# Kernel tuning notes

Measured on AMD Instinct MI355X. Metric: run time of the kernel, lower is better.

The kernel has to match this reference:

```python
import jax, jax.numpy as jnp
import numpy as np
from jax import lax

K = 3  # AdaConv kernel_size inside conv_block


def conv2d(x, w, b, pad):
    # x: (B,C,H,W), w: (O,I,kh,kw) -> NCHW conv with symmetric padding
    y = lax.conv_general_dilated(x, w, (1, 1), [(pad, pad), (pad, pad)],
                                 dimension_numbers=('NCHW', 'OIHW', 'NCHW'))
    return y + b[None, :, None, None]


def unfold3(x):
    # nn.Unfold(kernel=3, pad=1): patches ordered channel-major then (kh,kw) row-major
    B, C, H, W = x.shape
    xp = jnp.pad(x, ((0, 0), (0, 0), (1, 1), (1, 1)))
    return jnp.stack([xp[:, :, i:i + H, j:j + W]
                      for i in range(K) for j in range(K)], axis=2)  # (B,C,9,H,W)


def adaconv(x, mask, aw_w, aw_b, mt_w, mt_b, c_w, c_b):
    # groups=1, groups_channels=out_ch in this configuration
    weight = conv2d(mask, aw_w, aw_b, pad=2)          # (B, 9, H, W)
    x = conv2d(x, c_w, c_b, pad=1)                    # (B, out_ch, H, W)
    p = unfold3(x)                                    # (B, out_ch, 9, H, W)
    out = jnp.einsum('bkhw,bckhw->bchw', weight, p)   # per-pixel adaptive conv
    mask2 = conv2d(mask, mt_w, mt_b, pad=2)
    return out, mask2


def lrelu(x):
    return jax.nn.leaky_relu(x, 0.01)


def setup_inputs() -> dict:
    key = jax.random.key(0)
    ks = jax.random.split(key, 20)
    B, Cin, Cout, Mi, Mo, H, W = 2, 64, 64, 64, 64, 256, 256
    s = 0.05
    d = {
        'x': jax.random.normal(ks[0], (B, Cin, H, W), jnp.float32),
        'mask': jax.random.normal(ks[1], (B, Mi, H, W), jnp.float32),
        # AdaConv 1 (in_ch->out_ch, mask_in->mask_out)
        'aw1_w': jax.random.normal(ks[2], (K * K, Mi, 2 * K - 1, 2 * K - 1), jnp.float32) * s,
        'aw1_b': jax.random.normal(ks[3], (K * K,), jnp.float32) * s,
        'mt1_w': jax.random.normal(ks[4], (Mo, Mi, 2 * K - 1, 2 * K - 1), jnp.float32) * s,
        'mt1_b': jax.random.normal(ks[5], (Mo,), jnp.float32) * s,
        'c1_w': jax.random.normal(ks[6], (Cout, Cin, K, K), jnp.float32) * s,
        'c1_b': jax.random.normal(ks[7], (Cout,), jnp.float32) * s,
        # AdaConv 2 (out_ch->out_ch, mask_out->mask_out)
        'aw2_w': jax.random.normal(ks[8], (K * K, Mo, 2 * K - 1, 2 * K - 1), jnp.float32) * s,
        'aw2_b': jax.random.normal(ks[9], (K * K,), jnp.float32) * s,
        'mt2_w': jax.random.normal(ks[10], (Mo, Mo, 2 * K - 1, 2 * K - 1), jnp.float32) * s,
        'mt2_b': jax.random.normal(ks[11], (Mo,), jnp.float32) * s,
        'c2_w': jax.random.normal(ks[12], (Cout, Cout, K, K), jnp.float32) * s,
        'c2_b': jax.random.normal(ks[13], (Cout,), jnp.float32) * s,
        # 1x1 residual conv
        'cr_w': jax.random.normal(ks[14], (Cout, Cin, 1, 1), jnp.float32) * s,
        'cr_b': jax.random.normal(ks[15], (Cout,), jnp.float32) * s,
    }
    return d


def reference(x, mask, aw1_w, aw1_b, mt1_w, mt1_b, c1_w, c1_b,
              aw2_w, aw2_b, mt2_w, mt2_b, c2_w, c2_b, cr_w, cr_b):
    res = conv2d(x, cr_w, cr_b, pad=0)
    x, mask = adaconv(x, mask, aw1_w, aw1_b, mt1_w, mt1_b, c1_w, c1_b)
    x, mask = lrelu(x), lrelu(mask)
    x, mask = adaconv(x, mask, aw2_w, aw2_b, mt2_w, mt2_b, c2_w, c2_b)
    x, mask = lrelu(x), lrelu(mask)
    return (x + res, mask)
```

## Files before the change

kernel.cpp:

```cpp
#include <hip/hip_runtime.h>

#define HWSZ 65536
#define CCH  64

typedef __bf16 bf16x8 __attribute__((ext_vector_type(8)));
typedef __bf16 bf16x4 __attribute__((ext_vector_type(4)));
typedef float  f32x4  __attribute__((ext_vector_type(4)));

__device__ inline void gload_lds16(const void* g, void* l) {
    __builtin_amdgcn_global_load_lds(
        (const __attribute__((address_space(1))) void*)g,
        (__attribute__((address_space(3))) void*)l, 16, 0, 0);
}


__device__ void cvt_body(int cb, const float* __restrict__ src,
                         __bf16* __restrict__ dst)
{
    int p  = cb * 256 + threadIdx.x;
    int b  = p >> 16, hw = p & 65535;
    const float* sp = src + (((size_t)b * 64) << 16) + hw;
    __bf16* dp = dst + (size_t)p * 64;
    #pragma unroll
    for (int c8 = 0; c8 < 8; ++c8) {
        bf16x8 v8;
        #pragma unroll
        for (int j = 0; j < 8; ++j)
            v8[j] = (__bf16)sp[(size_t)(c8 * 8 + j) << 16];
        *(bf16x8*)(dp + c8 * 8) = v8;
    }
}

__device__ void prep3_body(int cb, const float* __restrict__ src,
                           __bf16* __restrict__ dst)
{
    int t = cb * 256 + threadIdx.x;
    if (t >= 2 * 9 * 2048) return;
    int j  = t & 7;
    int u  = (t >> 3) & 255;
    int q  = t >> 11;
    int k  = q % 9, ci = q / 9;
    int r  = u >> 3;
    int v  = (u & 7) ^ (r & 7);
    int o  = 2 * r + (v >> 2);
    int g  = v & 3;
    int i  = ci * 32 + g * 8 + j;
    dst[t] = (__bf16)src[((size_t)o * 64 + i) * 9 + k];
}

__device__ void prep1_body(int cb, const float* __restrict__ src,
                           __bf16* __restrict__ dst)
{
    int t = cb * 256 + threadIdx.x;
    if (t >= 2 * 2048) return;
    int j  = t & 7;
    int u  = (t >> 3) & 255;
    int ci = t >> 11;
    int r  = u >> 3;
    int v  = (u & 7) ^ (r & 7);
    int o  = 2 * r + (v >> 2);
    int g  = v & 3;
    int i  = ci * 32 + g * 8 + j;
    dst[t] = (__bf16)src[(size_t)o * 64 + i];
}

__device__ void prepF_body(int cb, const float* __restrict__ mt,
                           const float* __restrict__ aw, __bf16* __restrict__ dst)
{
    int t = cb * 256 + threadIdx.x;
    if (t >= 2 * 25 * 3072) return;
    int j  = t & 7;
    int u  = (t >> 3) % 384;
    int q  = t / 3072;
    int k  = q % 25, ci = q / 25;
    int r  = u >> 3;
    int v  = (u & 7) ^ (r & 7);
    int o  = 2 * r + (v >> 2);
    int g  = v & 3;
    int i  = ci * 32 + g * 8 + j;
    float val = 0.f;
    if (o < 64)      val = mt[((size_t)o * 64 + i) * 25 + k];
    else if (o < 73) val = aw[((size_t)(o - 64) * 64 + i) * 25 + k];
    dst[t] = (__bf16)val;
}

__global__ __launch_bounds__(256) void k_prep(
    const float* x, const float* mask,
    const float* c1w, const float* c2w,
    const float* mt1w, const float* aw1w,
    const float* mt2w, const float* aw2w,
    const float* crw,
    __bf16* xh, __bf16* mh,
    __bf16* wbc1, __bf16* wbc2, __bf16* wbF1, __bf16* wbF2, __bf16* wbcr)
{
    int bid = blockIdx.x;
    if      (bid < 512)  cvt_body(bid, x, xh);
    else if (bid < 1024) cvt_body(bid - 512, mask, mh);
    else if (bid < 1168) prep3_body(bid - 1024, c1w, wbc1);
    else if (bid < 1312) prep3_body(bid - 1168, c2w, wbc2);
    else if (bid < 1912) prepF_body(bid - 1312, mt1w, aw1w, wbF1);
    else if (bid < 2512) prepF_body(bid - 1912, mt2w, aw2w, wbF2);
    else                 prep1_body(bid - 2512, crw, wbcr);
}

template<int EPI>
__global__ __launch_bounds__(256) void k_conv5(
    const __bf16* __restrict__ xh, const __bf16* __restrict__ wb,
    const float* __restrict__ bias, const float* __restrict__ bias2,
    float* __restrict__ outf, __bf16* __restrict__ outh,
    float* __restrict__ out2)
{
    constexpr int TW    = 20;
    constexpr int NPIX  = 400;
    constexpr int KK    = 25;
    constexpr int SROWS = 96;
    constexpr int SLICE = SROWS * 64;
    constexpr int NPIX2 = NPIX / 2;
    constexpr int MFT   = 5;

    __shared__ __align__(16) __bf16 lx[NPIX2 * 64];
    __shared__ __align__(16) __bf16 lw[2][SROWS * 32];
    __shared__ float lb[80];

    const int t    = threadIdx.x;
    const int w0   = blockIdx.x * 16, h0 = blockIdx.y * 16, b = blockIdx.z;
    const int wvv  = t >> 6;
    const int lane = t & 63;
    const int px   = lane & 15;
    const int g    = lane >> 4;

    auto STAGE = [&](int ci, int k, int buf) {
        const char* gs = (const char*)wb + (size_t)(ci * KK + k) * SLICE;
        if (wvv < 3) {
            #pragma unroll
            for (int r = 0; r < 2; ++r) {
                int ub = wvv * 128 + r * 64;
                gload_lds16(gs + (ub + lane) * 16, (char*)lw[buf] + ub * 16);
            }
        }
    };

    f32x4 acc[MFT][4];
    #pragma unroll
    for (int m = 0; m < MFT; ++m)
        #pragma unroll
        for (int nf = 0; nf < 4; ++nf)
            acc[m][nf] = (f32x4){0.f, 0.f, 0.f, 0.f};

    bf16x8 zv;
    #pragma unroll
    for (int j = 0; j < 8; ++j) zv[j] = (__bf16)0.f;

    for (int ci = 0; ci < 2; ++ci) {
        if (ci) __syncthreads();
        STAGE(ci, 0, 0);
        STAGE(ci, 1, 1);
        if (ci == 0) {
            if (t < 64) lb[t] = bias[t];
            if (t >= 64 && t < 80) lb[t] = (t - 64 < 9) ? bias2[t - 64] : 0.f;
        }

        #pragma unroll
        for (int xi = 0; xi < 7; ++xi) {
            int e = xi * 256 + t;
            if (e < NPIX * 4) {
                int pix = e >> 2, c4 = e & 3;
                int sy = pix / TW, sx = pix - sy * TW;
                int gy = h0 + sy - 2, gx = w0 + sx - 2;
                bool ok = (unsigned)gy < 256u && (unsigned)gx < 256u;
                bf16x8 v8 = zv;
                if (ok) v8 = *(const bf16x8*)(xh + ((((size_t)b << 16) + gy * 256 + gx) << 6)
                                              + ci * 32 + c4 * 8);
                int row = pix >> 1;
                int off = row * 128 + (((((pix & 1) << 2) + c4) ^ (row & 7)) << 4);
                *(bf16x8*)((char*)lx + off) = v8;
            }
        }
        __syncthreads();

        #pragma unroll
        for (int k = 0; k < KK; ++k) {
            const __bf16* lwb = (k & 1) ? lw[1] : lw[0];
            const int dy = k / 5, dx = k - dy * 5;

            bf16x8 bfr[4];
            #pragma unroll
            for (int nf = 0; nf < 4; ++nf) {
                int pix = (wvv * 4 + nf + dy) * TW + (px + dx);
                int row = pix >> 1;
                int off = row * 128 + (((((pix & 1) << 2) + g) ^ (row & 7)) << 4);
                bfr[nf] = *(const bf16x8*)((const char*)lx + off);
            }
            bf16x8 afr[MFT];
            #pragma unroll
            for (int m = 0; m < MFT; ++m) {
                int o = m * 16 + px;
                int row = o >> 1;
                int off = row * 128 + (((((o & 1) << 2) + g) ^ (row & 7)) << 4);
                afr[m] = *(const bf16x8*)((const char*)lwb + off);
            }
            __builtin_amdgcn_s_setprio(1);
            #pragma unroll
            for (int m = 0; m < MFT; ++m)
                #pragma unroll
                for (int nf = 0; nf < 4; ++nf)
                    acc[m][nf] = __builtin_amdgcn_mfma_f32_16x16x32_bf16(
                        afr[m], bfr[nf], acc[m][nf], 0, 0, 0);
            __builtin_amdgcn_s_setprio(0);

            if (k == KK - 1) break;

            asm volatile("s_waitcnt lgkmcnt(0)" ::: "memory");
            __builtin_amdgcn_sched_barrier(0);
            __builtin_amdgcn_s_barrier();
            bool issued = (k + 2 < KK);
            if (issued) STAGE(ci, k + 2, k & 1);
            if (issued && wvv < 3) asm volatile("s_waitcnt vmcnt(2)" ::: "memory");
            else                   asm volatile("s_waitcnt vmcnt(0)" ::: "memory");
            __builtin_amdgcn_sched_barrier(0);
            __builtin_amdgcn_s_barrier();
        }
    }

    #pragma unroll
    for (int m = 0; m < MFT; ++m) {
        #pragma unroll
        for (int nf = 0; nf < 4; ++nf) {
            int row = h0 + wvv * 4 + nf, col = w0 + px;
            if (m < 4) {
                float vj[4];
                #pragma unroll
                for (int j = 0; j < 4; ++j) {
                    float v = acc[m][nf][j] + lb[m * 16 + g * 4 + j];
                    vj[j] = v > 0.f ? v : 0.01f * v;
                }
                if constexpr (EPI == 0) {
                    bf16x4 pk;
                    #pragma unroll
                    for (int j = 0; j < 4; ++j) pk[j] = (__bf16)vj[j];
                    *(bf16x4*)(outh + ((((size_t)b << 16) + row * 256 + col) << 6)
                                    + m * 16 + g * 4) = pk;
                } else {
                    #pragma unroll
                    for (int j = 0; j < 4; ++j)
                        outf[((size_t)(b * 64 + m * 16 + g * 4 + j) << 16)
                             + row * 256 + col] = vj[j];
                }
            } else {
                #pragma unroll
                for (int j = 0; j < 4; ++j) {
                    int o2 = g * 4 + j;
                    if (o2 < 9)
                        out2[((size_t)(b * 9 + o2) << 16) + row * 256 + col]
                            = acc[m][nf][j] + lb[64 + o2];
                }
            }
        }
    }
}

__global__ __launch_bounds__(256) void k_conv3(
    const __bf16* __restrict__ xh, const __bf16* __restrict__ wb,
    const float* __restrict__ bias, __bf16* __restrict__ outh)
{
    constexpr int TW    = 18;
    constexpr int NPIX  = 324;
    constexpr int NPIX2 = 162;

    __shared__ __align__(16) __bf16 lx[NPIX2 * 64];
    __shared__ __align__(16) __bf16 lw[9 * 2048];
    __shared__ float lb[64];

    const int t    = threadIdx.x;
    const int w0   = blockIdx.x * 16, h0 = blockIdx.y * 16, b = blockIdx.z;
    const int wvv  = t >> 6;
    const int lane = t & 63;
    const int px   = lane & 15;
    const int g    = lane >> 4;

    f32x4 acc[4][4];
    #pragma unroll
    for (int m = 0; m < 4; ++m)
        #pragma unroll
        for (int nf = 0; nf < 4; ++nf)
            acc[m][nf] = (f32x4){0.f, 0.f, 0.f, 0.f};

    bf16x8 zv;
    #pragma unroll
    for (int j = 0; j < 8; ++j) zv[j] = (__bf16)0.f;

    for (int ci = 0; ci < 2; ++ci) {
        if (ci) __syncthreads();
        {
            const char* gs = (const char*)wb + (size_t)ci * 9 * 4096;
            #pragma unroll
            for (int r = 0; r < 9; ++r) {
                int ub = r * 256 + wvv * 64;
                gload_lds16(gs + (ub + lane) * 16, (char*)lw + ub * 16);
            }
        }
        if (ci == 0 && t < 64) lb[t] = bias[t];

        #pragma unroll
        for (int xi = 0; xi < 6; ++xi) {
            int e = xi * 256 + t;
            if (e < NPIX * 4) {
                int pix = e >> 2, c4 = e & 3;
                int sy = pix / TW, sx = pix - sy * TW;
                int gy = h0 + sy - 1, gx = w0 + sx - 1;
                bool ok = (unsigned)gy < 256u && (unsigned)gx < 256u;
                bf16x8 v8 = zv;
                if (ok) v8 = *(const bf16x8*)(xh + ((((size_t)b << 16) + gy * 256 + gx) << 6)
                                              + ci * 32 + c4 * 8);
                int row = pix >> 1;
                int off = row * 128 + (((((pix & 1) << 2) + c4) ^ (row & 7)) << 4);
                *(bf16x8*)((char*)lx + off) = v8;
            }
        }
        __syncthreads();

        #pragma unroll
        for (int k = 0; k < 9; ++k) {
            const __bf16* lwb = lw + k * 2048;
            const int dy = k / 3, dx = k - dy * 3;

            bf16x8 bfr[4];
            #pragma unroll
            for (int nf = 0; nf < 4; ++nf) {
                int pix = (wvv * 4 + nf + dy) * TW + (px + dx);
                int row = pix >> 1;
                int off = row * 128 + (((((pix & 1) << 2) + g) ^ (row & 7)) << 4);
                bfr[nf] = *(const bf16x8*)((const char*)lx + off);
            }
            bf16x8 afr[4];
            #pragma unroll
            for (int m = 0; m < 4; ++m) {
                int o = m * 16 + px;
                int row = o >> 1;
                int off = row * 128 + (((((o & 1) << 2) + g) ^ (row & 7)) << 4);
                afr[m] = *(const bf16x8*)((const char*)lwb + off);
            }
            __builtin_amdgcn_s_setprio(1);
            #pragma unroll
            for (int m = 0; m < 4; ++m)
                #pragma unroll
                for (int nf = 0; nf < 4; ++nf)
                    acc[m][nf] = __builtin_amdgcn_mfma_f32_16x16x32_bf16(
                        afr[m], bfr[nf], acc[m][nf], 0, 0, 0);
            __builtin_amdgcn_s_setprio(0);
        }
    }

    #pragma unroll
    for (int m = 0; m < 4; ++m) {
        #pragma unroll
        for (int nf = 0; nf < 4; ++nf) {
            int row = h0 + wvv * 4 + nf, col = w0 + px;
            bf16x4 pk;
            #pragma unroll
            for (int j = 0; j < 4; ++j) {
                float v = acc[m][nf][j] + lb[m * 16 + g * 4 + j];
                pk[j] = (__bf16)v;
            }
            *(bf16x4*)(outh + ((((size_t)b << 16) + row * 256 + col) << 6)
                            + m * 16 + g * 4) = pk;
        }
    }
}

__global__ __launch_bounds__(256) void k_conv1(
    const __bf16* __restrict__ xh, const __bf16* __restrict__ wb,
    const float* __restrict__ bias, __bf16* __restrict__ outh)
{
    constexpr int NPIX2 = 128;

    __shared__ __align__(16) __bf16 lx[NPIX2 * 64];
    __shared__ __align__(16) __bf16 lw[2048];
    __shared__ float lb[64];

    const int t    = threadIdx.x;
    const int w0   = blockIdx.x * 16, h0 = blockIdx.y * 16, b = blockIdx.z;
    const int wvv  = t >> 6;
    const int lane = t & 63;
    const int px   = lane & 15;
    const int g    = lane >> 4;

    f32x4 acc[4][4];
    #pragma unroll
    for (int m = 0; m < 4; ++m)
        #pragma unroll
        for (int nf = 0; nf < 4; ++nf)
            acc[m][nf] = (f32x4){0.f, 0.f, 0.f, 0.f};

    for (int ci = 0; ci < 2; ++ci) {
        if (ci) __syncthreads();
        {
            const char* gs = (const char*)wb + (size_t)ci * 4096;
            int ub = wvv * 64;
            gload_lds16(gs + (ub + lane) * 16, (char*)lw + ub * 16);
        }
        if (ci == 0 && t < 64) lb[t] = bias[t];

        #pragma unroll
        for (int xi = 0; xi < 4; ++xi) {
            int e = xi * 256 + t;
            int pix = e >> 2, c4 = e & 3;
            int gy = h0 + (pix >> 4), gx = w0 + (pix & 15);
            bf16x8 v8 = *(const bf16x8*)(xh + ((((size_t)b << 16) + gy * 256 + gx) << 6)
                                         + ci * 32 + c4 * 8);
            int row = pix >> 1;
            int off = row * 128 + (((((pix & 1) << 2) + c4) ^ (row & 7)) << 4);
            *(bf16x8*)((char*)lx + off) = v8;
        }
        __syncthreads();

        bf16x8 bfr[4];
        #pragma unroll
        for (int nf = 0; nf < 4; ++nf) {
            int pix = (wvv * 4 + nf) * 16 + px;
            int row = pix >> 1;
            int off = row * 128 + (((((pix & 1) << 2) + g) ^ (row & 7)) << 4);
            bfr[nf] = *(const bf16x8*)((const char*)lx + off);
        }
        bf16x8 afr[4];
        #pragma unroll
        for (int m = 0; m < 4; ++m) {
            int o = m * 16 + px;
            int row = o >> 1;
            int off = row * 128 + (((((o & 1) << 2) + g) ^ (row & 7)) << 4);
            afr[m] = *(const bf16x8*)((const char*)lw + off);
        }
        #pragma unroll
        for (int m = 0; m < 4; ++m)
            #pragma unroll
            for (int nf = 0; nf < 4; ++nf)
                acc[m][nf] = __builtin_amdgcn_mfma_f32_16x16x32_bf16(
                    afr[m], bfr[nf], acc[m][nf], 0, 0, 0);
    }

    #pragma unroll
    for (int m = 0; m < 4; ++m) {
        #pragma unroll
        for (int nf = 0; nf < 4; ++nf) {
            int row = h0 + wvv * 4 + nf, col = w0 + px;
            bf16x4 pk;
            #pragma unroll
            for (int j = 0; j < 4; ++j)
                pk[j] = (__bf16)(acc[m][nf][j] + lb[m * 16 + g * 4 + j]);
            *(bf16x4*)(outh + ((((size_t)b << 16) + row * 256 + col) << 6)
                            + m * 16 + g * 4) = pk;
        }
    }
}

__global__ __launch_bounds__(256, 4) void k_ada1(
    const float* __restrict__ wgt, const __bf16* __restrict__ xin,
    __bf16* __restrict__ outh)
{
    int t  = threadIdx.x;
    int pg = t >> 3, c8 = t & 7;
    int p  = blockIdx.x * 32 + pg;
    int b  = p >> 16, hw = p & 65535;
    int h  = hw >> 8, wc = hw & 255;

    const float* wp = wgt + ((size_t)(b * 9) << 16) + hw;
    const __bf16* cen = xin + (size_t)p * 64 + c8 * 8;

    float wk[9];
    const __bf16* nbp[9];
    #pragma unroll
    for (int dy = 0; dy < 3; ++dy)
        #pragma unroll
        for (int dx = 0; dx < 3; ++dx) {
            int k = dy * 3 + dx;
            bool ok = ((unsigned)(h + dy - 1) < 256u) &&
                      ((unsigned)(wc + dx - 1) < 256u);
            wk[k]  = ok ? wp[(size_t)k << 16] : 0.f;
            nbp[k] = ok ? cen + ((dy - 1) * 256 + (dx - 1)) * 64 : cen;
        }

    float acc[8] = {0.f,0.f,0.f,0.f,0.f,0.f,0.f,0.f};
    #pragma unroll
    for (int k = 0; k < 9; ++k) {
        bf16x8 v8 = *(const bf16x8*)nbp[k];
        float w = wk[k];
        #pragma unroll
        for (int j = 0; j < 8; ++j) acc[j] += w * (float)v8[j];
    }

    bf16x8 o8;
    #pragma unroll
    for (int j = 0; j < 8; ++j) {
        float v = acc[j];
        o8[j] = (__bf16)(v > 0.f ? v : 0.01f * v);
    }
    *(bf16x8*)(outh + (size_t)p * 64 + c8 * 8) = o8;
}

__global__ __launch_bounds__(256, 4) void k_ada2(
    const float* __restrict__ wgt, const __bf16* __restrict__ x2h,
    const __bf16* __restrict__ resh, float* __restrict__ outf)
{
    __shared__ float ls[32 * 65];

    int t  = threadIdx.x;
    int pg = t >> 3, c8 = t & 7;
    int p  = blockIdx.x * 32 + pg;
    int b  = p >> 16, hw = p & 65535;
    int h  = hw >> 8, wc = hw & 255;

    const float* wp = wgt + ((size_t)(b * 9) << 16) + hw;
    const __bf16* cen = x2h + (size_t)p * 64 + c8 * 8;

    float wk[9];
    const __bf16* nbp[9];
    #pragma unroll
    for (int dy = 0; dy < 3; ++dy)
        #pragma unroll
        for (int dx = 0; dx < 3; ++dx) {
            int k = dy * 3 + dx;
            bool ok = ((unsigned)(h + dy - 1) < 256u) &&
                      ((unsigned)(wc + dx - 1) < 256u);
            wk[k]  = ok ? wp[(size_t)k << 16] : 0.f;
            nbp[k] = ok ? cen + ((dy - 1) * 256 + (dx - 1)) * 64 : cen;
        }

    float acc[8] = {0.f,0.f,0.f,0.f,0.f,0.f,0.f,0.f};
    #pragma unroll
    for (int k = 0; k < 9; ++k) {
        bf16x8 v8 = *(const bf16x8*)nbp[k];
        float w = wk[k];
        #pragma unroll
        for (int j = 0; j < 8; ++j) acc[j] += w * (float)v8[j];
    }

    bf16x8 r8 = *(const bf16x8*)(resh + (size_t)p * 64 + c8 * 8);
    #pragma unroll
    for (int j = 0; j < 8; ++j) {
        float v = acc[j];
        v = v > 0.f ? v : 0.01f * v;
        ls[pg * 65 + c8 * 8 + j] = v + (float)r8[j];
    }
    __syncthreads();

    int pbase = blockIdx.x * 32;
    int bb    = pbase >> 16, hwb = pbase & 65535;
    int pix   = t & 31, cq = t >> 5;
    #pragma unroll
    for (int i = 0; i < 8; ++i) {
        int c = i * 8 + cq;
        size_t oi = ((size_t)(bb * 64 + c) << 16) + hwb + pix;
        outf[oi] = ls[pix * 65 + c];
    }
}

extern "C" void kernel_launch(void* const* d_in, const int* in_sizes, int n_in,
                              void* d_out, int out_size, void* d_ws, size_t ws_size,
                              hipStream_t stream)
{
    const float* x     = (const float*)d_in[0];
    const float* mask  = (const float*)d_in[1];
    const float* aw1_w = (const float*)d_in[2];
    const float* aw1_b = (const float*)d_in[3];
    const float* mt1_w = (const float*)d_in[4];
    const float* mt1_b = (const float*)d_in[5];
    const float* c1_w  = (const float*)d_in[6];
    const float* c1_b  = (const float*)d_in[7];
    const float* aw2_w = (const float*)d_in[8];
    const float* aw2_b = (const float*)d_in[9];
    const float* mt2_w = (const float*)d_in[10];
    const float* mt2_b = (const float*)d_in[11];
    const float* c2_w  = (const float*)d_in[12];
    const float* c2_b  = (const float*)d_in[13];
    const float* cr_w  = (const float*)d_in[14];
    const float* cr_b  = (const float*)d_in[15];

    float* out_x = (float*)d_out;
    float* out_m = (float*)d_out + 8388608;

    float*  wgt   = (float*)d_ws;
    __bf16* xh    = (__bf16*)((char*)d_ws + 4718592);
    __bf16* mh    = (__bf16*)((char*)d_ws + 21495808);
    __bf16* x2h   = mh;
    __bf16* wbase = (__bf16*)((char*)d_ws + 38273024);
    __bf16* wb_c1 = wbase;
    __bf16* wb_c2 = wbase + 36864;
    __bf16* wb_F1 = wbase + 73728;
    __bf16* wb_F2 = wbase + 227328;
    __bf16* wb_cr = wbase + 380928;
    __bf16* resh  = (__bf16*)((char*)d_ws + 39043072);

    __bf16* maska_h = (__bf16*)out_x;
    __bf16* xa_h    = (__bf16*)out_x + 8388608;
    __bf16* x1_h    = (__bf16*)out_m;

    dim3 blk(256);
    dim3 gconv(16, 16, 2);
    dim3 gada(4096);

    k_prep<<<dim3(2528), blk, 0, stream>>>(x, mask, c1_w, c2_w,
        mt1_w, aw1_w, mt2_w, aw2_w, cr_w,
        xh, mh, wb_c1, wb_c2, wb_F1, wb_F2, wb_cr);

    k_conv5<0><<<gconv, blk, 0, stream>>>(mh, wb_F1, mt1_b, aw1_b,
                                          nullptr, maska_h, wgt);
    k_conv3<<<gconv, blk, 0, stream>>>(xh, wb_c1, c1_b, x1_h);
    k_ada1<<<gada, blk, 0, stream>>>(wgt, x1_h, xa_h);
    k_conv5<1><<<gconv, blk, 0, stream>>>(maska_h, wb_F2, mt2_b, aw2_b,
                                          out_m, nullptr, wgt);
    k_conv3<<<gconv, blk, 0, stream>>>(xa_h, wb_c2, c2_b, x2h);
    k_conv1<<<gconv, blk, 0, stream>>>(xh, wb_cr, cr_b, resh);
    k_ada2<<<gada, blk, 0, stream>>>(wgt, x2h, resh, out_x);
}
```

Before: 169.3 us.

## Reorder conv taps column-major to reuse input fragments across dy and stage weights per column

The prep kernels now permute 3x3 and 5x5 weight slices so taps are stored column-major (dx outer, dy inner). The 5x5 and 3x3 conv loops load one column of input fragments (4+dy rows) once per dx and reuse them across all dy taps, which cuts LDS reads of the activation tile. In the 5x5 kernel the two-slice double buffer is replaced by a single buffer holding all five dy weight slices of a column group. That means fewer barriers per channel half, but LDS use rises and the next group's load is only overlapped with the MFMA loop after the weights are pulled into registers. Register pressure goes up: the 5x5 loop holds 25 A fragments plus 9 B fragments.

```diff
diff --git a/kernel.cpp b/kernel.cpp
--- a/kernel.cpp
+++ b/kernel.cpp
@@ -39,7 +39,9 @@
     int j  = t & 7;
     int u  = (t >> 3) & 255;
     int q  = t >> 11;
-    int k  = q % 9, ci = q / 9;
+    int s  = q % 9, ci = q / 9;
+    int dx = s / 3, dy = s % 3;
+    int k  = dy * 3 + dx;
     int r  = u >> 3;
     int v  = (u & 7) ^ (r & 7);
     int o  = 2 * r + (v >> 2);
@@ -72,7 +74,9 @@
     int j  = t & 7;
     int u  = (t >> 3) % 384;
     int q  = t / 3072;
-    int k  = q % 25, ci = q / 25;
+    int s  = q % 25, ci = q / 25;
+    int dx = s / 5, dy = s % 5;
+    int k  = dy * 5 + dx;
     int r  = u >> 3;
     int v  = (u & 7) ^ (r & 7);
     int o  = 2 * r + (v >> 2);
@@ -112,14 +116,12 @@
 {
     constexpr int TW    = 20;
     constexpr int NPIX  = 400;
-    constexpr int KK    = 25;
-    constexpr int SROWS = 96;
-    constexpr int SLICE = SROWS * 64;
     constexpr int NPIX2 = NPIX / 2;
     constexpr int MFT   = 5;
+    constexpr int SLICE = 6144;
 
     __shared__ __align__(16) __bf16 lx[NPIX2 * 64];
-    __shared__ __align__(16) __bf16 lw[2][SROWS * 32];
+    __shared__ __align__(16) __bf16 lw[5 * 3072];
     __shared__ float lb[80];
 
     const int t    = threadIdx.x;
@@ -129,14 +131,13 @@
     const int px   = lane & 15;
     const int g    = lane >> 4;
 
-    auto STAGE = [&](int ci, int k, int buf) {
-        const char* gs = (const char*)wb + (size_t)(ci * KK + k) * SLICE;
-        if (wvv < 3) {
-            #pragma unroll
-            for (int r = 0; r < 2; ++r) {
-                int ub = wvv * 128 + r * 64;
-                gload_lds16(gs + (ub + lane) * 16, (char*)lw[buf] + ub * 16);
-            }
+    auto STAGE_GRP = [&](int ci, int grp) {
+        const char* gs = (const char*)wb + (size_t)(ci * 25 + grp * 5) * SLICE;
+        #pragma unroll
+        for (int r = 0; r < 8; ++r) {
+            int u = r * 256 + wvv * 64;
+            if (u < 1920)
+                gload_lds16(gs + (u + lane) * 16, (char*)lw + u * 16);
         }
     };
 
@@ -152,9 +153,7 @@
     for (int j = 0; j < 8; ++j) zv[j] = (__bf16)0.f;
 
     for (int ci = 0; ci < 2; ++ci) {
-        if (ci) __syncthreads();
-        STAGE(ci, 0, 0);
-        STAGE(ci, 1, 1);
+        STAGE_GRP(ci, 0);
         if (ci == 0) {
             if (t < 64) lb[t] = bias[t];
             if (t >= 64 && t < 80) lb[t] = (t - 64 < 9) ? bias2[t - 64] : 0.f;
@@ -179,44 +178,45 @@
         __syncthreads();
 
         #pragma unroll
-        for (int k = 0; k < KK; ++k) {
-            const __bf16* lwb = (k & 1) ? lw[1] : lw[0];
-            const int dy = k / 5, dx = k - dy * 5;
-
-            bf16x8 bfr[4];
-            #pragma unroll
-            for (int nf = 0; nf < 4; ++nf) {
-                int pix = (wvv * 4 + nf + dy) * TW + (px + dx);
+        for (int dxg = 0; dxg < 5; ++dxg) {
+            bf16x8 bfr[9];
+            #pragma unroll
+            for (int r = 0; r < 9; ++r) {
+                int pix = (wvv * 4 + r) * TW + (px + dxg);
                 int row = pix >> 1;
                 int off = row * 128 + (((((pix & 1) << 2) + g) ^ (row & 7)) << 4);
-                bfr[nf] = *(const bf16x8*)((const char*)lx + off);
-            }
-            bf16x8 afr[MFT];
-            #pragma unroll
-            for (int m = 0; m < MFT; ++m) {
-                int o = m * 16 + px;
-                int row = o >> 1;
-                int off = row * 128 + (((((o & 1) << 2) + g) ^ (row & 7)) << 4);
-                afr[m] = *(const bf16x8*)((const char*)lwb + off);
-            }
-            __builtin_amdgcn_s_setprio(1);
-            #pragma unroll
-            for (int m = 0; m < MFT; ++m)
+                bfr[r] = *(const bf16x8*)((const char*)lx + off);
+            }
+            bf16x8 afr[5][MFT];
+            #pragma unroll
+            for (int dy = 0; dy < 5; ++dy)
                 #pragma unroll
-                for (int nf = 0; nf < 4; ++nf)
-                    acc[m][nf] = __builtin_amdgcn_mfma_f32_16x16x32_bf16(
-                        afr[m], bfr[nf], acc[m][nf], 0, 0, 0);
-            __builtin_amdgcn_s_setprio(0);
-
-            if (k == KK - 1) break;
+                for (int m = 0; m < MFT; ++m) {
+                    int o = m * 16 + px;
+                    int row = o >> 1;
+                    int off = dy * SLICE + row * 128
+                            + (((((o & 1) << 2) + g) ^ (row & 7)) << 4);
+                    afr[dy][m] = *(const bf16x8*)((const char*)lw + off);
+                }
 
             asm volatile("s_waitcnt lgkmcnt(0)" ::: "memory");
             __builtin_amdgcn_sched_barrier(0);
             __builtin_amdgcn_s_barrier();
-            bool issued = (k + 2 < KK);
-            if (issued) STAGE(ci, k + 2, k & 1);
-            if (issued && wvv < 3) asm volatile("s_waitcnt vmcnt(2)" ::: "memory");
-            else                   asm volatile("s_waitcnt vmcnt(0)" ::: "memory");
+
+            if (dxg < 4) STAGE_GRP(ci, dxg + 1);
+
+            __builtin_amdgcn_s_setprio(1);
+            #pragma unroll
+            for (int dy = 0; dy < 5; ++dy)
+                #pragma unroll
+                for (int m = 0; m < MFT; ++m)
+                    #pragma unroll
+                    for (int nf = 0; nf < 4; ++nf)
+                        acc[m][nf] = __builtin_amdgcn_mfma_f32_16x16x32_bf16(
+                            afr[dy][m], bfr[nf + dy], acc[m][nf], 0, 0, 0);
+            __builtin_amdgcn_s_setprio(0);
+
+            asm volatile("s_waitcnt vmcnt(0)" ::: "memory");
             __builtin_amdgcn_sched_barrier(0);
             __builtin_amdgcn_s_barrier();
         }
@@ -320,34 +320,35 @@
         __syncthreads();
 
         #pragma unroll
-        for (int k = 0; k < 9; ++k) {
-            const __bf16* lwb = lw + k * 2048;
-            const int dy = k / 3, dx = k - dy * 3;
-
-            bf16x8 bfr[4];
-            #pragma unroll
-            for (int nf = 0; nf < 4; ++nf) {
-                int pix = (wvv * 4 + nf + dy) * TW + (px + dx);
+        for (int dxg = 0; dxg < 3; ++dxg) {
+            bf16x8 bfr[6];
+            #pragma unroll
+            for (int r = 0; r < 6; ++r) {
+                int pix = (wvv * 4 + r) * TW + (px + dxg);
                 int row = pix >> 1;
                 int off = row * 128 + (((((pix & 1) << 2) + g) ^ (row & 7)) << 4);
-                bfr[nf] = *(const bf16x8*)((const char*)lx + off);
-            }
-            bf16x8 afr[4];
-            #pragma unroll
-            for (int m = 0; m < 4; ++m) {
-                int o = m * 16 + px;
-                int row = o >> 1;
-                int off = row * 128 + (((((o & 1) << 2) + g) ^ (row & 7)) << 4);
-                afr[m] = *(const bf16x8*)((const char*)lwb + off);
-            }
-            __builtin_amdgcn_s_setprio(1);
-            #pragma unroll
-            for (int m = 0; m < 4; ++m)
+                bfr[r] = *(const bf16x8*)((const char*)lx + off);
+            }
+            #pragma unroll
+            for (int dy = 0; dy < 3; ++dy) {
+                const __bf16* lwb = lw + (dxg * 3 + dy) * 2048;
+                bf16x8 afr[4];
                 #pragma unroll
-                for (int nf = 0; nf < 4; ++nf)
-                    acc[m][nf] = __builtin_amdgcn_mfma_f32_16x16x32_bf16(
-                        afr[m], bfr[nf], acc[m][nf], 0, 0, 0);
-            __builtin_amdgcn_s_setprio(0);
+                for (int m = 0; m < 4; ++m) {
+                    int o = m * 16 + px;
+                    int row = o >> 1;
+                    int off = row * 128 + (((((o & 1) << 2) + g) ^ (row & 7)) << 4);
+                    afr[m] = *(const bf16x8*)((const char*)lwb + off);
+                }
+                __builtin_amdgcn_s_setprio(1);
+                #pragma unroll
+                for (int m = 0; m < 4; ++m)
+                    #pragma unroll
+                    for (int nf = 0; nf < 4; ++nf)
+                        acc[m][nf] = __builtin_amdgcn_mfma_f32_16x16x32_bf16(
+                            afr[m], bfr[nf + dy], acc[m][nf], 0, 0, 0);
+                __builtin_amdgcn_s_setprio(0);
+            }
         }
     }
 
```

Measured after the change: 178.5 us. 1.05x slower.
